# Optimization experiments

Measured on AMD Instinct MI355X. Metric: run time of the kernel, lower is better.

## Reference

```python
import jax, jax.numpy as jnp
import numpy as np

N, H, W = 1024, 256, 256
EPS2D = 0.3  # gsplat low-pass filter on 2D covariance

C0 = 0.28209479177387814
C1 = 0.4886025119029199
C2 = (1.0925484305920792, -1.0925484305920792, 0.31539156525252005, -1.0925484305920792, 0.5462742152960396)
C3 = (-0.5900435899266435, 2.890611442640554, -0.4570457994644658, 0.3731763325901154, -0.4570457994644658, 1.445305721320277, -0.5900435899266435)


def setup_inputs() -> dict:
    key = jax.random.key(0)
    ks = jax.random.split(key, 9)
    means = jax.random.normal(ks[0], (N, 3), jnp.float32)
    scales = jax.random.normal(ks[1], (N, 3), jnp.float32) * 0.3 - 3.0  # exp -> ~0.05
    quats = jax.random.normal(ks[2], (N, 4), jnp.float32)
    opacities = jax.random.normal(ks[3], (N, 1), jnp.float32)
    sh_0 = jax.random.normal(ks[4], (N, 1, 3), jnp.float32) * 0.5
    sh_n = jax.random.normal(ks[5], (N, 15, 3), jnp.float32) * 0.1
    times = jax.random.uniform(ks[6], (N, 1), jnp.float32)
    durations = jax.random.normal(ks[7], (N, 1), jnp.float32) * 0.5
    velocities = jax.random.normal(ks[8], (N, 3), jnp.float32) * 0.1
    # camera: identity rotation, points pushed to depth ~5 in front
    w2c = jnp.eye(4, dtype=jnp.float32).at[2, 3].set(5.0)[None]
    intrinsic = jnp.array([[[300.0, 0.0, 128.0], [0.0, 300.0, 128.0], [0.0, 0.0, 1.0]]], jnp.float32)
    return {"means": means, "scales": scales, "quats": quats, "opacities": opacities,
            "sh_0": sh_0, "sh_n": sh_n, "times": times, "durations": durations,
            "velocities": velocities, "t": jnp.float32(0.5), "w2c": w2c,
            "intrinsic": intrinsic, "height": H, "width": W}


def _quat_to_rot(q):
    q = q / jnp.linalg.norm(q, axis=-1, keepdims=True)
    w, x, y, z = q[:, 0], q[:, 1], q[:, 2], q[:, 3]
    R = jnp.stack([
        1 - 2 * (y * y + z * z), 2 * (x * y - w * z), 2 * (x * z + w * y),
        2 * (x * y + w * z), 1 - 2 * (x * x + z * z), 2 * (y * z - w * x),
        2 * (x * z - w * y), 2 * (y * z + w * x), 1 - 2 * (x * x + y * y),
    ], axis=-1).reshape(-1, 3, 3)
    return R


def _sh_colors(sh, dirs):
    # sh: [N,16,3], dirs: [N,3] normalized. Real SH up to degree 3 (gsplat convention).
    x, y, z = dirs[:, 0], dirs[:, 1], dirs[:, 2]
    xx, yy, zz = x * x, y * y, z * z
    basis = jnp.stack([
        jnp.full_like(x, C0),
        -C1 * y, C1 * z, -C1 * x,
        C2[0] * x * y, C2[1] * y * z, C2[2] * (2 * zz - xx - yy), C2[3] * x * z, C2[4] * (xx - yy),
        C3[0] * y * (3 * xx - yy), C3[1] * x * y * z, C3[2] * y * (4 * zz - xx - yy),
        C3[3] * z * (2 * zz - 3 * xx - 3 * yy), C3[4] * x * (4 * zz - xx - yy),
        C3[5] * z * (xx - yy), C3[6] * x * (xx - 3 * yy),
    ], axis=-1)  # [N,16]
    return jnp.maximum(jnp.einsum('nk,nkc->nc', basis, sh) + 0.5, 0.0)


def reference(means, scales, quats, opacities, sh_0, sh_n, times, durations, velocities,
              t, w2c, intrinsic, height, width):
    # temporal updates
    means_t = means + (t - times) * velocities                                   # [N,3]
    opac = (jax.nn.sigmoid(opacities) * jnp.exp(-0.5 * ((t - times) / jnp.exp(durations)) ** 2))[:, 0]
    sig = jnp.exp(scales)                                                        # [N,3]

    Rcw, tcw = w2c[0, :3, :3], w2c[0, :3, 3]
    K = intrinsic[0]
    fx, fy, cx, cy = K[0, 0], K[1, 1], K[0, 2], K[1, 2]

    # project means
    p_cam = means_t @ Rcw.T + tcw                                                # [N,3]
    zc = p_cam[:, 2]
    u = fx * p_cam[:, 0] / zc + cx
    v = fy * p_cam[:, 1] / zc + cy

    # 3D covariance in camera frame
    Rg = _quat_to_rot(quats)                                                     # [N,3,3]
    M = Rg * sig[:, None, :]
    cov3d = jnp.einsum('nij,nkj->nik', M, M)
    cov_cam = jnp.einsum('ij,njk,lk->nil', Rcw, cov3d, Rcw)

    # perspective Jacobian -> 2D covariance (EWA)
    zero = jnp.zeros_like(zc)
    J = jnp.stack([
        jnp.stack([fx / zc, zero, -fx * p_cam[:, 0] / zc ** 2], -1),
        jnp.stack([zero, fy / zc, -fy * p_cam[:, 1] / zc ** 2], -1),
    ], axis=1)                                                                   # [N,2,3]
    cov2d = jnp.einsum('nij,njk,nlk->nil', J, cov_cam, J)
    a = cov2d[:, 0, 0] + EPS2D
    b = cov2d[:, 0, 1]
    c = cov2d[:, 1, 1] + EPS2D
    det = a * c - b * b
    conA, conB, conC = c / det, -b / det, a / det

    # colors from SH
    cam_pos = -Rcw.T @ tcw
    dirs = means_t - cam_pos
    dirs = dirs / jnp.linalg.norm(dirs, axis=-1, keepdims=True)
    colors = _sh_colors(jnp.concatenate([sh_0, sh_n], axis=1), dirs)             # [N,3]

    # dense per-pixel gaussian evaluation (pixel centers at +0.5)
    xs = jnp.arange(width, dtype=jnp.float32) + 0.5
    ys = jnp.arange(height, dtype=jnp.float32) + 0.5
    gx, gy = jnp.meshgrid(xs, ys)                                                # [H,W]
    px, py = gx.reshape(-1), gy.reshape(-1)                                      # [HW]
    dx = px[None, :] - u[:, None]                                                # [N,HW]
    dy = py[None, :] - v[:, None]
    sigma = 0.5 * (conA[:, None] * dx * dx + conC[:, None] * dy * dy) + conB[:, None] * dx * dy
    valid = (zc > 0.01) & (det > 1e-12)
    alpha = jnp.minimum(0.999, opac[:, None] * jnp.exp(-jnp.maximum(sigma, 0.0)))
    alpha = jnp.where(valid[:, None] & (sigma >= 0.0) & (alpha >= 1.0 / 255.0), alpha, 0.0)

    # depth sort, front-to-back alpha compositing
    order = jnp.argsort(zc)
    alpha_s = alpha[order]
    colors_s = colors[order]
    Tcum = jnp.cumprod(1.0 - alpha_s, axis=0)                                    # [N,HW]
    T_excl = jnp.concatenate([jnp.ones((1, alpha_s.shape[1]), alpha_s.dtype), Tcum[:-1]], axis=0)
    w = alpha_s * T_excl                                                         # [N,HW]
    image = jnp.einsum('np,nc->pc', w, colors_s).reshape(1, height, width, 3)
    alpha_out = (1.0 - Tcum[-1]).reshape(1, height, width, 1)
    image = jnp.clip(image, 0.0, 1.0)
    return image, alpha_out
```

## Files before the change

kernel.cpp:

```cpp
#include <hip/hip_runtime.h>
#include <math.h>

#define NG 1024
#define IH 256
#define IW 256
#define NPIX (IH*IW)


__global__ __launch_bounds__(64) void k_pre(
    const float* __restrict__ means, const float* __restrict__ scales,
    const float* __restrict__ quats, const float* __restrict__ opacs,
    const float* __restrict__ sh0, const float* __restrict__ shn,
    const float* __restrict__ times, const float* __restrict__ durs,
    const float* __restrict__ vels, const float* __restrict__ tptr,
    const float* __restrict__ w2c, const float* __restrict__ intr,
    float* __restrict__ zc_out, float* __restrict__ raw)
{
    int g = blockIdx.x * 64 + threadIdx.x;
    if (g >= NG) return;
    const float t = tptr[0];
    const float R00=w2c[0], R01=w2c[1], R02=w2c[2],  tx=w2c[3];
    const float R10=w2c[4], R11=w2c[5], R12=w2c[6],  ty=w2c[7];
    const float R20=w2c[8], R21=w2c[9], R22=w2c[10], tz=w2c[11];
    const float fx=intr[0], cx=intr[2], fy=intr[4], cy=intr[5];

    const float dt = t - times[g];
    const float mx = fmaf(dt, vels[g*3+0], means[g*3+0]);
    const float my = fmaf(dt, vels[g*3+1], means[g*3+1]);
    const float mz = fmaf(dt, vels[g*3+2], means[g*3+2]);

    const float o = opacs[g];
    const float sig_o = 1.f / (1.f + __expf(-o));
    const float ratio = dt * __expf(-durs[g]);
    const float opac = sig_o * __expf(-0.5f * ratio * ratio);

    const float xc = R00*mx + R01*my + R02*mz + tx;
    const float yc = R10*mx + R11*my + R12*mz + ty;
    const float zc = R20*mx + R21*my + R22*mz + tz;
    const float iz = 1.f / zc;
    const float u = fx*xc*iz + cx;
    const float v = fy*yc*iz + cy;

    float qw=quats[g*4+0], qx=quats[g*4+1], qy=quats[g*4+2], qz=quats[g*4+3];
    const float qn = rsqrtf(qw*qw + qx*qx + qy*qy + qz*qz);
    qw*=qn; qx*=qn; qy*=qn; qz*=qn;
    const float sx = __expf(scales[g*3+0]);
    const float sy = __expf(scales[g*3+1]);
    const float sz = __expf(scales[g*3+2]);
    const float G00 = 1.f-2.f*(qy*qy+qz*qz), G01 = 2.f*(qx*qy-qw*qz), G02 = 2.f*(qx*qz+qw*qy);
    const float G10 = 2.f*(qx*qy+qw*qz), G11 = 1.f-2.f*(qx*qx+qz*qz), G12 = 2.f*(qy*qz-qw*qx);
    const float G20 = 2.f*(qx*qz-qw*qy), G21 = 2.f*(qy*qz+qw*qx), G22 = 1.f-2.f*(qx*qx+qy*qy);
    const float M00=G00*sx, M01=G01*sy, M02=G02*sz;
    const float M10=G10*sx, M11=G11*sy, M12=G12*sz;
    const float M20=G20*sx, M21=G21*sy, M22=G22*sz;
    const float W00=R00*M00+R01*M10+R02*M20, W01=R00*M01+R01*M11+R02*M21, W02=R00*M02+R01*M12+R02*M22;
    const float W10=R10*M00+R11*M10+R12*M20, W11=R10*M01+R11*M11+R12*M21, W12=R10*M02+R11*M12+R12*M22;
    const float W20=R20*M00+R21*M10+R22*M20, W21=R20*M01+R21*M11+R22*M21, W22=R20*M02+R21*M12+R22*M22;
    const float xdz = xc*iz, ydz = yc*iz;
    const float fxiz = fx*iz, fyiz = fy*iz;
    const float T00 = fxiz*(W00 - xdz*W20), T01 = fxiz*(W01 - xdz*W21), T02 = fxiz*(W02 - xdz*W22);
    const float T10 = fyiz*(W10 - ydz*W20), T11 = fyiz*(W11 - ydz*W21), T12 = fyiz*(W12 - ydz*W22);
    const float a = T00*T00 + T01*T01 + T02*T02 + 0.3f;
    const float b = T00*T10 + T01*T11 + T02*T12;
    const float c = T10*T10 + T11*T11 + T12*T12 + 0.3f;
    const float det = a*c - b*b;
    const float idet = 1.f / det;
    const float conA = c*idet, conB = -b*idet, conC = a*idet;

    const bool valid = (zc > 0.01f) && (det > 1e-12f);
    const float op_eff = valid ? opac : 0.f;
    const float smax = (op_eff * 255.f > 0.f) ? (logf(op_eff * 255.f) + 1e-4f) : -1e30f;
    float rx, ry;
    if (smax > 0.f) {
        rx = sqrtf(2.f * smax * a) + 0.01f;
        ry = sqrtf(2.f * smax * c) + 0.01f;
    } else {
        rx = -1e30f; ry = -1e30f;
    }

    const float cpx = -(R00*tx + R10*ty + R20*tz);
    const float cpy = -(R01*tx + R11*ty + R21*tz);
    const float cpz = -(R02*tx + R12*ty + R22*tz);
    float dx0 = mx-cpx, dy0 = my-cpy, dz0 = mz-cpz;
    const float dn = rsqrtf(dx0*dx0 + dy0*dy0 + dz0*dz0);
    const float X = dx0*dn, Y = dy0*dn, Z = dz0*dn;
    const float XX=X*X, YY=Y*Y, ZZ=Z*Z;

    float bs[16];
    bs[0]  = 0.28209479177387814f;
    bs[1]  = -0.4886025119029199f * Y;
    bs[2]  =  0.4886025119029199f * Z;
    bs[3]  = -0.4886025119029199f * X;
    bs[4]  =  1.0925484305920792f * X * Y;
    bs[5]  = -1.0925484305920792f * Y * Z;
    bs[6]  =  0.31539156525252005f * (2.f*ZZ - XX - YY);
    bs[7]  = -1.0925484305920792f * X * Z;
    bs[8]  =  0.5462742152960396f * (XX - YY);
    bs[9]  = -0.5900435899266435f * Y * (3.f*XX - YY);
    bs[10] =  2.890611442640554f  * X * Y * Z;
    bs[11] = -0.4570457994644658f * Y * (4.f*ZZ - XX - YY);
    bs[12] =  0.3731763325901154f * Z * (2.f*ZZ - 3.f*XX - 3.f*YY);
    bs[13] = -0.4570457994644658f * X * (4.f*ZZ - XX - YY);
    bs[14] =  1.445305721320277f  * Z * (XX - YY);
    bs[15] = -0.5900435899266435f * X * (XX - 3.f*YY);

    float cr = 0.5f, cg = 0.5f, cb = 0.5f;
    cr = fmaf(bs[0], sh0[g*3+0], cr);
    cg = fmaf(bs[0], sh0[g*3+1], cg);
    cb = fmaf(bs[0], sh0[g*3+2], cb);
    #pragma unroll
    for (int k = 1; k < 16; ++k) {
        const float* s = shn + g*45 + (k-1)*3;
        cr = fmaf(bs[k], s[0], cr);
        cg = fmaf(bs[k], s[1], cg);
        cb = fmaf(bs[k], s[2], cb);
    }
    cr = fmaxf(cr, 0.f); cg = fmaxf(cg, 0.f); cb = fmaxf(cb, 0.f);

    zc_out[g] = zc;
    float* r = raw + g*12;
    r[0] = u;         r[1] = v;    r[2]  = rx;       r[3]  = ry;
    r[4] = 0.5f*conA; r[5] = conB; r[6]  = 0.5f*conC;r[7]  = smax;
    r[8] = op_eff;    r[9] = cr;   r[10] = cg;       r[11] = cb;
}

__global__ __launch_bounds__(64) void k_rank(
    const float* __restrict__ zc, const float* __restrict__ raw,
    float* __restrict__ sorted)
{
    const int g = blockIdx.x;
    const int lane = threadIdx.x;
    const float myz = zc[g];
    int cnt = 0;
    #pragma unroll
    for (int k = 0; k < 16; ++k) {
        const int j = k*64 + lane;
        const float z = zc[j];
        const bool lt = (z < myz) || (z == myz && j < g);
        cnt += (int)__popcll(__ballot(lt));
    }
    if (lane < 12) sorted[cnt*12 + lane] = raw[g*12 + lane];
}

__global__ __launch_bounds__(256) void k_raster(
    const float* __restrict__ sorted, float* __restrict__ out)
{
    __shared__ float4 hrec[4][64][3];
    __shared__ float4 part[4][64];
    const int lane = threadIdx.x & 63;
    const int wv   = threadIdx.x >> 6;
    const int pix  = blockIdx.x * 64 + lane;
    const float px = (float)(pix & (IW-1)) + 0.5f;
    const float py = (float)(pix >> 8) + 0.5f;
    const float px0  = (float)((blockIdx.x & 3) << 6) + 0.5f;
    const float px63 = px0 + 63.f;

    const float4* __restrict__ gp = (const float4*)sorted;
    const int base = wv * 256;

    unsigned long long masks[4];
    #pragma unroll
    for (int k = 0; k < 4; ++k) {
        const float4 r0 = gp[(base + k*64 + lane)*3];
        masks[k] = __ballot((fabsf(py - r0.y) <= r0.w) &&
                            (r0.x + r0.z >= px0) && (r0.x - r0.z <= px63));
    }

    float T = 1.f, cr = 0.f, cg = 0.f, cb = 0.f;
    #pragma unroll
    for (int k = 0; k < 4; ++k) {
        const unsigned long long m = masks[k];
        if (!m) continue;
        const int g = base + k*64 + lane;
        if ((m >> lane) & 1ull) {
            const int pos = (int)__popcll(m & ((1ull << lane) - 1ull));
            hrec[wv][pos][0] = gp[g*3+0];
            hrec[wv][pos][1] = gp[g*3+1];
            hrec[wv][pos][2] = gp[g*3+2];
        }
        asm volatile("s_waitcnt lgkmcnt(0)" ::: "memory");
        const int cnt = (int)__popcll(m);
        for (int i = 0; i < cnt; ++i) {
            const float4 ra = hrec[wv][i][0];
            const float4 rb = hrec[wv][i][1];
            const float4 rc = hrec[wv][i][2];
            const float dx = px - ra.x;
            const float dy = py - ra.y;
            const float sigma = fmaf(dx, fmaf(rb.x, dx, rb.y*dy), rb.z*dy*dy);
            if (sigma >= 0.f && sigma <= rb.w) {
                const float al = fminf(0.999f, rc.x * __expf(-sigma));
                if (al >= (1.f/255.f)) {
                    const float w = al * T;
                    cr = fmaf(w, rc.y, cr);
                    cg = fmaf(w, rc.z, cg);
                    cb = fmaf(w, rc.w, cb);
                    T -= w;
                }
            }
        }
    }

    part[wv][lane] = make_float4(cr, cg, cb, T);
    __syncthreads();
    if (threadIdx.x < 64) {
        const float4 v0 = part[0][lane];
        const float4 v1 = part[1][lane];
        const float4 v2 = part[2][lane];
        const float4 v3 = part[3][lane];
        float r = v0.x, g2 = v0.y, b2 = v0.z, Tt = v0.w;
        r = fmaf(Tt, v1.x, r); g2 = fmaf(Tt, v1.y, g2); b2 = fmaf(Tt, v1.z, b2); Tt *= v1.w;
        r = fmaf(Tt, v2.x, r); g2 = fmaf(Tt, v2.y, g2); b2 = fmaf(Tt, v2.z, b2); Tt *= v2.w;
        r = fmaf(Tt, v3.x, r); g2 = fmaf(Tt, v3.y, g2); b2 = fmaf(Tt, v3.z, b2); Tt *= v3.w;
        const int p3 = pix * 3;
        out[p3+0] = fminf(fmaxf(r,  0.f), 1.f);
        out[p3+1] = fminf(fmaxf(g2, 0.f), 1.f);
        out[p3+2] = fminf(fmaxf(b2, 0.f), 1.f);
        out[NPIX*3 + pix] = 1.f - Tt;
    }
}

extern "C" void kernel_launch(void* const* d_in, const int* in_sizes, int n_in,
                              void* d_out, int out_size, void* d_ws, size_t ws_size,
                              hipStream_t stream) {
    const float* means  = (const float*)d_in[0];
    const float* scales = (const float*)d_in[1];
    const float* quats  = (const float*)d_in[2];
    const float* opacs  = (const float*)d_in[3];
    const float* sh0    = (const float*)d_in[4];
    const float* shn    = (const float*)d_in[5];
    const float* times  = (const float*)d_in[6];
    const float* durs   = (const float*)d_in[7];
    const float* vels   = (const float*)d_in[8];
    const float* tptr   = (const float*)d_in[9];
    const float* w2c    = (const float*)d_in[10];
    const float* intr   = (const float*)d_in[11];

    float* ws     = (float*)d_ws;
    float* zc     = ws;
    float* raw    = ws + 1024;
    float* sorted = ws + 1024 + 12*NG;

    hipLaunchKernelGGL(k_pre, dim3(16), dim3(64), 0, stream,
                       means, scales, quats, opacs, sh0, shn,
                       times, durs, vels, tptr, w2c, intr, zc, raw);
    hipLaunchKernelGGL(k_rank, dim3(NG), dim3(64), 0, stream, zc, raw, sorted);
    hipLaunchKernelGGL(k_raster, dim3(NPIX/64), dim3(256), 0, stream,
                       sorted, (float*)d_out);
}
```

Measured before the change: 19.94 us.

## Drop global sort kernel; sort per-block culled gaussians in shared memory

Removes the separate k_rank launch that globally sorted all gaussians by depth. Instead, each raster block culls gaussians against its 64-pixel row, gathers the survivors into shared memory and ranks them there by depth with an O(H^2) count. The sorted list is split evenly across the four waves, which balances work between waves. The shared list is capped at 192 entries, so rows with more overlapping gaussians silently drop some, which risks incorrect output. Every block also repeats the sort, adding per-block overhead in exchange for one fewer kernel launch.

```diff
diff --git a/kernel.cpp b/kernel.cpp
--- a/kernel.cpp
+++ b/kernel.cpp
@@ -5,6 +5,7 @@
 #define IH 256
 #define IW 256
 #define NPIX (IH*IW)
+#define CAP 192
 
 
 __global__ __launch_bounds__(64) void k_pre(
@@ -119,34 +120,22 @@
 
     zc_out[g] = zc;
     float* r = raw + g*12;
-    r[0] = u;         r[1] = v;    r[2]  = rx;       r[3]  = ry;
-    r[4] = 0.5f*conA; r[5] = conB; r[6]  = 0.5f*conC;r[7]  = smax;
-    r[8] = op_eff;    r[9] = cr;   r[10] = cg;       r[11] = cb;
+    r[0] = u;         r[1] = v;    r[2]  = rx;        r[3]  = ry;
+    r[4] = 0.5f*conA; r[5] = conB; r[6]  = 0.5f*conC; r[7]  = smax;
+    r[8] = op_eff;    r[9] = cr;   r[10] = cg;        r[11] = cb;
 }
 
-__global__ __launch_bounds__(64) void k_rank(
-    const float* __restrict__ zc, const float* __restrict__ raw,
-    float* __restrict__ sorted)
+__global__ __launch_bounds__(256) void k_raster(
+    const float* __restrict__ raw, const float* __restrict__ zc,
+    float* __restrict__ out)
 {
-    const int g = blockIdx.x;
-    const int lane = threadIdx.x;
-    const float myz = zc[g];
-    int cnt = 0;
-    #pragma unroll
-    for (int k = 0; k < 16; ++k) {
-        const int j = k*64 + lane;
-        const float z = zc[j];
-        const bool lt = (z < myz) || (z == myz && j < g);
-        cnt += (int)__popcll(__ballot(lt));
-    }
-    if (lane < 12) sorted[cnt*12 + lane] = raw[g*12 + lane];
-}
-
-__global__ __launch_bounds__(256) void k_raster(
-    const float* __restrict__ sorted, float* __restrict__ out)
-{
-    __shared__ float4 hrec[4][64][3];
+    __shared__ float4 hrec[CAP][3];
+    __shared__ float  hz[CAP];
+    __shared__ int    hid[CAP];
+    __shared__ int    hperm[CAP];
+    __shared__ int    cnts[4];
     __shared__ float4 part[4][64];
+
     const int lane = threadIdx.x & 63;
     const int wv   = threadIdx.x >> 6;
     const int pix  = blockIdx.x * 64 + lane;
@@ -155,47 +144,82 @@
     const float px0  = (float)((blockIdx.x & 3) << 6) + 0.5f;
     const float px63 = px0 + 63.f;
 
-    const float4* __restrict__ gp = (const float4*)sorted;
+    const float4* __restrict__ gp = (const float4*)raw;
     const int base = wv * 256;
 
+    float4 r0s[4];
     unsigned long long masks[4];
     #pragma unroll
     for (int k = 0; k < 4; ++k) {
         const float4 r0 = gp[(base + k*64 + lane)*3];
+        r0s[k] = r0;
         masks[k] = __ballot((fabsf(py - r0.y) <= r0.w) &&
                             (r0.x + r0.z >= px0) && (r0.x - r0.z <= px63));
     }
-
-    float T = 1.f, cr = 0.f, cg = 0.f, cb = 0.f;
+    const int cw = (int)(__popcll(masks[0]) + __popcll(masks[1]) +
+                         __popcll(masks[2]) + __popcll(masks[3]));
+    if (lane == 0) cnts[wv] = cw;
+    __syncthreads();
+
+    int off = 0;
+    #pragma unroll
+    for (int w = 0; w < 4; ++w) off += (w < wv) ? cnts[w] : 0;
+    const int tot = cnts[0] + cnts[1] + cnts[2] + cnts[3];
+
+    int pbase = off;
     #pragma unroll
     for (int k = 0; k < 4; ++k) {
         const unsigned long long m = masks[k];
-        if (!m) continue;
-        const int g = base + k*64 + lane;
         if ((m >> lane) & 1ull) {
-            const int pos = (int)__popcll(m & ((1ull << lane) - 1ull));
-            hrec[wv][pos][0] = gp[g*3+0];
-            hrec[wv][pos][1] = gp[g*3+1];
-            hrec[wv][pos][2] = gp[g*3+2];
+            const int pos = pbase + (int)__popcll(m & ((1ull << lane) - 1ull));
+            if (pos < CAP) {
+                const int g = base + k*64 + lane;
+                hrec[pos][0] = r0s[k];
+                hrec[pos][1] = gp[g*3+1];
+                hrec[pos][2] = gp[g*3+2];
+                hz[pos] = zc[g];
+                hid[pos] = g;
+            }
         }
-        asm volatile("s_waitcnt lgkmcnt(0)" ::: "memory");
-        const int cnt = (int)__popcll(m);
-        for (int i = 0; i < cnt; ++i) {
-            const float4 ra = hrec[wv][i][0];
-            const float4 rb = hrec[wv][i][1];
-            const float4 rc = hrec[wv][i][2];
-            const float dx = px - ra.x;
-            const float dy = py - ra.y;
-            const float sigma = fmaf(dx, fmaf(rb.x, dx, rb.y*dy), rb.z*dy*dy);
-            if (sigma >= 0.f && sigma <= rb.w) {
-                const float al = fminf(0.999f, rc.x * __expf(-sigma));
-                if (al >= (1.f/255.f)) {
-                    const float w = al * T;
-                    cr = fmaf(w, rc.y, cr);
-                    cg = fmaf(w, rc.z, cg);
-                    cb = fmaf(w, rc.w, cb);
-                    T -= w;
-                }
+        pbase += (int)__popcll(m);
+    }
+    __syncthreads();
+
+    const int H = (tot < CAP) ? tot : CAP;
+
+    for (int t = threadIdx.x; t < H; t += 256) {
+        const float zt = hz[t];
+        const int   it = hid[t];
+        int r = 0;
+        for (int j = 0; j < H; ++j) {
+            const float zj = hz[j];
+            const int   ij = hid[j];
+            r += (zj < zt) || (zj == zt && ij < it);
+        }
+        hperm[r] = t;
+    }
+    __syncthreads();
+
+    const int Q = (H + 3) >> 2;
+    const int s = wv * Q;
+    const int e = (s + Q < H) ? (s + Q) : H;
+    float T = 1.f, cr = 0.f, cg = 0.f, cb = 0.f;
+    for (int i = s; i < e; ++i) {
+        const int p = hperm[i];
+        const float4 ra = hrec[p][0];
+        const float4 rb = hrec[p][1];
+        const float4 rc = hrec[p][2];
+        const float dx = px - ra.x;
+        const float dy = py - ra.y;
+        const float sigma = fmaf(dx, fmaf(rb.x, dx, rb.y*dy), rb.z*dy*dy);
+        if (sigma >= 0.f && sigma <= rb.w) {
+            const float al = fminf(0.999f, rc.x * __expf(-sigma));
+            if (al >= (1.f/255.f)) {
+                const float w = al * T;
+                cr = fmaf(w, rc.y, cr);
+                cg = fmaf(w, rc.z, cg);
+                cb = fmaf(w, rc.w, cb);
+                T -= w;
             }
         }
     }
@@ -235,15 +259,13 @@
     const float* w2c    = (const float*)d_in[10];
     const float* intr   = (const float*)d_in[11];
 
-    float* ws     = (float*)d_ws;
-    float* zc     = ws;
-    float* raw    = ws + 1024;
-    float* sorted = ws + 1024 + 12*NG;
+    float* ws  = (float*)d_ws;
+    float* zc  = ws;
+    float* raw = ws + 1024;
 
     hipLaunchKernelGGL(k_pre, dim3(16), dim3(64), 0, stream,
                        means, scales, quats, opacs, sh0, shn,
                        times, durs, vels, tptr, w2c, intr, zc, raw);
-    hipLaunchKernelGGL(k_rank, dim3(NG), dim3(64), 0, stream, zc, raw, sorted);
     hipLaunchKernelGGL(k_raster, dim3(NPIX/64), dim3(256), 0, stream,
-                       sorted, (float*)d_out);
+                       raw, zc, (float*)d_out);
 }
```

Result: slower. 23.87 us (+19.7%).

## Fuse depth ranking into preprocessing kernel and split culling records

Applied to the files above, without the earlier changes.

Each preprocessing block now recomputes all 1024 camera-space depths into shared memory and ranks its own 64 gaussians there. Three waves count over depth chunks while one wave does the projection and SH work. The separate rank kernel and its launch go away, and records are scattered directly in sorted order. The cull fields move to their own float4 array, which the raster kernel keeps in registers, and the per-gaussian LDS record loads are software-pipelined one step ahead. In exchange, every block redundantly reloads means, velocities and times for all gaussians.

```diff
diff --git a/kernel.cpp b/kernel.cpp
--- a/kernel.cpp
+++ b/kernel.cpp
@@ -7,143 +7,175 @@
 #define NPIX (IH*IW)
 
 
-__global__ __launch_bounds__(64) void k_pre(
+__global__ __launch_bounds__(256) void k_pre(
     const float* __restrict__ means, const float* __restrict__ scales,
     const float* __restrict__ quats, const float* __restrict__ opacs,
     const float* __restrict__ sh0, const float* __restrict__ shn,
     const float* __restrict__ times, const float* __restrict__ durs,
     const float* __restrict__ vels, const float* __restrict__ tptr,
     const float* __restrict__ w2c, const float* __restrict__ intr,
-    float* __restrict__ zc_out, float* __restrict__ raw)
+    float* __restrict__ cull, float* __restrict__ recs)
 {
-    int g = blockIdx.x * 64 + threadIdx.x;
-    if (g >= NG) return;
+    __shared__ float zall[NG];
+    __shared__ int   partial[4][64];
+
+    const int tid = threadIdx.x;
+    const int b   = blockIdx.x;
     const float t = tptr[0];
     const float R00=w2c[0], R01=w2c[1], R02=w2c[2],  tx=w2c[3];
     const float R10=w2c[4], R11=w2c[5], R12=w2c[6],  ty=w2c[7];
     const float R20=w2c[8], R21=w2c[9], R22=w2c[10], tz=w2c[11];
     const float fx=intr[0], cx=intr[2], fy=intr[4], cy=intr[5];
 
-    const float dt = t - times[g];
-    const float mx = fmaf(dt, vels[g*3+0], means[g*3+0]);
-    const float my = fmaf(dt, vels[g*3+1], means[g*3+1]);
-    const float mz = fmaf(dt, vels[g*3+2], means[g*3+2]);
-
-    const float o = opacs[g];
-    const float sig_o = 1.f / (1.f + __expf(-o));
-    const float ratio = dt * __expf(-durs[g]);
-    const float opac = sig_o * __expf(-0.5f * ratio * ratio);
-
-    const float xc = R00*mx + R01*my + R02*mz + tx;
-    const float yc = R10*mx + R11*my + R12*mz + ty;
-    const float zc = R20*mx + R21*my + R22*mz + tz;
-    const float iz = 1.f / zc;
-    const float u = fx*xc*iz + cx;
-    const float v = fy*yc*iz + cy;
-
-    float qw=quats[g*4+0], qx=quats[g*4+1], qy=quats[g*4+2], qz=quats[g*4+3];
-    const float qn = rsqrtf(qw*qw + qx*qx + qy*qy + qz*qz);
-    qw*=qn; qx*=qn; qy*=qn; qz*=qn;
-    const float sx = __expf(scales[g*3+0]);
-    const float sy = __expf(scales[g*3+1]);
-    const float sz = __expf(scales[g*3+2]);
-    const float G00 = 1.f-2.f*(qy*qy+qz*qz), G01 = 2.f*(qx*qy-qw*qz), G02 = 2.f*(qx*qz+qw*qy);
-    const float G10 = 2.f*(qx*qy+qw*qz), G11 = 1.f-2.f*(qx*qx+qz*qz), G12 = 2.f*(qy*qz-qw*qx);
-    const float G20 = 2.f*(qx*qz-qw*qy), G21 = 2.f*(qy*qz+qw*qx), G22 = 1.f-2.f*(qx*qx+qy*qy);
-    const float M00=G00*sx, M01=G01*sy, M02=G02*sz;
-    const float M10=G10*sx, M11=G11*sy, M12=G12*sz;
-    const float M20=G20*sx, M21=G21*sy, M22=G22*sz;
-    const float W00=R00*M00+R01*M10+R02*M20, W01=R00*M01+R01*M11+R02*M21, W02=R00*M02+R01*M12+R02*M22;
-    const float W10=R10*M00+R11*M10+R12*M20, W11=R10*M01+R11*M11+R12*M21, W12=R10*M02+R11*M12+R12*M22;
-    const float W20=R20*M00+R21*M10+R22*M20, W21=R20*M01+R21*M11+R22*M21, W22=R20*M02+R21*M12+R22*M22;
-    const float xdz = xc*iz, ydz = yc*iz;
-    const float fxiz = fx*iz, fyiz = fy*iz;
-    const float T00 = fxiz*(W00 - xdz*W20), T01 = fxiz*(W01 - xdz*W21), T02 = fxiz*(W02 - xdz*W22);
-    const float T10 = fyiz*(W10 - ydz*W20), T11 = fyiz*(W11 - ydz*W21), T12 = fyiz*(W12 - ydz*W22);
-    const float a = T00*T00 + T01*T01 + T02*T02 + 0.3f;
-    const float b = T00*T10 + T01*T11 + T02*T12;
-    const float c = T10*T10 + T11*T11 + T12*T12 + 0.3f;
-    const float det = a*c - b*b;
-    const float idet = 1.f / det;
-    const float conA = c*idet, conB = -b*idet, conC = a*idet;
-
-    const bool valid = (zc > 0.01f) && (det > 1e-12f);
-    const float op_eff = valid ? opac : 0.f;
-    const float smax = (op_eff * 255.f > 0.f) ? (logf(op_eff * 255.f) + 1e-4f) : -1e30f;
-    float rx, ry;
-    if (smax > 0.f) {
-        rx = sqrtf(2.f * smax * a) + 0.01f;
-        ry = sqrtf(2.f * smax * c) + 0.01f;
+    #pragma unroll
+    for (int k = 0; k < 4; ++k) {
+        const int g = tid + k*256;
+        const float dt = t - times[g];
+        const float mx = fmaf(dt, vels[g*3+0], means[g*3+0]);
+        const float my = fmaf(dt, vels[g*3+1], means[g*3+1]);
+        const float mz = fmaf(dt, vels[g*3+2], means[g*3+2]);
+        zall[g] = R20*mx + R21*my + R22*mz + tz;
+    }
+    __syncthreads();
+
+    float o_u=0, o_v=0, o_rx=0, o_ry=0, o_hA=0, o_B=0, o_hC=0, o_smax=0;
+    float o_op=0, o_cr=0, o_cg=0, o_cb=0;
+    if (tid < 64) {
+        const int g = b*64 + tid;
+        const float dt = t - times[g];
+        const float mx = fmaf(dt, vels[g*3+0], means[g*3+0]);
+        const float my = fmaf(dt, vels[g*3+1], means[g*3+1]);
+        const float mz = fmaf(dt, vels[g*3+2], means[g*3+2]);
+
+        const float o = opacs[g];
+        const float sig_o = 1.f / (1.f + __expf(-o));
+        const float ratio = dt * __expf(-durs[g]);
+        const float opac = sig_o * __expf(-0.5f * ratio * ratio);
+
+        const float xc = R00*mx + R01*my + R02*mz + tx;
+        const float yc = R10*mx + R11*my + R12*mz + ty;
+        const float zc = R20*mx + R21*my + R22*mz + tz;
+        const float iz = 1.f / zc;
+        const float u = fx*xc*iz + cx;
+        const float v = fy*yc*iz + cy;
+
+        float qw=quats[g*4+0], qx=quats[g*4+1], qy=quats[g*4+2], qz=quats[g*4+3];
+        const float qn = rsqrtf(qw*qw + qx*qx + qy*qy + qz*qz);
+        qw*=qn; qx*=qn; qy*=qn; qz*=qn;
+        const float sx = __expf(scales[g*3+0]);
+        const float sy = __expf(scales[g*3+1]);
+        const float sz = __expf(scales[g*3+2]);
+        const float G00 = 1.f-2.f*(qy*qy+qz*qz), G01 = 2.f*(qx*qy-qw*qz), G02 = 2.f*(qx*qz+qw*qy);
+        const float G10 = 2.f*(qx*qy+qw*qz), G11 = 1.f-2.f*(qx*qx+qz*qz), G12 = 2.f*(qy*qz-qw*qx);
+        const float G20 = 2.f*(qx*qz-qw*qy), G21 = 2.f*(qy*qz+qw*qx), G22 = 1.f-2.f*(qx*qx+qy*qy);
+        const float M00=G00*sx, M01=G01*sy, M02=G02*sz;
+        const float M10=G10*sx, M11=G11*sy, M12=G12*sz;
+        const float M20=G20*sx, M21=G21*sy, M22=G22*sz;
+        const float W00=R00*M00+R01*M10+R02*M20, W01=R00*M01+R01*M11+R02*M21, W02=R00*M02+R01*M12+R02*M22;
+        const float W10=R10*M00+R11*M10+R12*M20, W11=R10*M01+R11*M11+R12*M21, W12=R10*M02+R11*M12+R12*M22;
+        const float W20=R20*M00+R21*M10+R22*M20, W21=R20*M01+R21*M11+R22*M21, W22=R20*M02+R21*M12+R22*M22;
+        const float xdz = xc*iz, ydz = yc*iz;
+        const float fxiz = fx*iz, fyiz = fy*iz;
+        const float T00 = fxiz*(W00 - xdz*W20), T01 = fxiz*(W01 - xdz*W21), T02 = fxiz*(W02 - xdz*W22);
+        const float T10 = fyiz*(W10 - ydz*W20), T11 = fyiz*(W11 - ydz*W21), T12 = fyiz*(W12 - ydz*W22);
+        const float a = T00*T00 + T01*T01 + T02*T02 + 0.3f;
+        const float bb = T00*T10 + T01*T11 + T02*T12;
+        const float c = T10*T10 + T11*T11 + T12*T12 + 0.3f;
+        const float det = a*c - bb*bb;
+        const float idet = 1.f / det;
+        const float conA = c*idet, conB = -bb*idet, conC = a*idet;
+
+        const bool valid = (zc > 0.01f) && (det > 1e-12f);
+        const float op_eff = valid ? opac : 0.f;
+        const float smax = (op_eff * 255.f > 0.f) ? (logf(op_eff * 255.f) + 1e-4f) : -1e30f;
+        float rx, ry;
+        if (smax > 0.f) {
+            rx = sqrtf(2.f * smax * a) + 0.01f;
+            ry = sqrtf(2.f * smax * c) + 0.01f;
+        } else {
+            rx = -1e30f; ry = -1e30f;
+        }
+
+        const float cpx = -(R00*tx + R10*ty + R20*tz);
+        const float cpy = -(R01*tx + R11*ty + R21*tz);
+        const float cpz = -(R02*tx + R12*ty + R22*tz);
+        float dx0 = mx-cpx, dy0 = my-cpy, dz0 = mz-cpz;
+        const float dn = rsqrtf(dx0*dx0 + dy0*dy0 + dz0*dz0);
+        const float X = dx0*dn, Y = dy0*dn, Z = dz0*dn;
+        const float XX=X*X, YY=Y*Y, ZZ=Z*Z;
+
+        float bs[16];
+        bs[0]  = 0.28209479177387814f;
+        bs[1]  = -0.4886025119029199f * Y;
+        bs[2]  =  0.4886025119029199f * Z;
+        bs[3]  = -0.4886025119029199f * X;
+        bs[4]  =  1.0925484305920792f * X * Y;
+        bs[5]  = -1.0925484305920792f * Y * Z;
+        bs[6]  =  0.31539156525252005f * (2.f*ZZ - XX - YY);
+        bs[7]  = -1.0925484305920792f * X * Z;
+        bs[8]  =  0.5462742152960396f * (XX - YY);
+        bs[9]  = -0.5900435899266435f * Y * (3.f*XX - YY);
+        bs[10] =  2.890611442640554f  * X * Y * Z;
+        bs[11] = -0.4570457994644658f * Y * (4.f*ZZ - XX - YY);
+        bs[12] =  0.3731763325901154f * Z * (2.f*ZZ - 3.f*XX - 3.f*YY);
+        bs[13] = -0.4570457994644658f * X * (4.f*ZZ - XX - YY);
+        bs[14] =  1.445305721320277f  * Z * (XX - YY);
+        bs[15] = -0.5900435899266435f * X * (XX - 3.f*YY);
+
+        float cr = 0.5f, cg = 0.5f, cb = 0.5f;
+        cr = fmaf(bs[0], sh0[g*3+0], cr);
+        cg = fmaf(bs[0], sh0[g*3+1], cg);
+        cb = fmaf(bs[0], sh0[g*3+2], cb);
+        #pragma unroll
+        for (int k = 1; k < 16; ++k) {
+            const float* s = shn + g*45 + (k-1)*3;
+            cr = fmaf(bs[k], s[0], cr);
+            cg = fmaf(bs[k], s[1], cg);
+            cb = fmaf(bs[k], s[2], cb);
+        }
+        cr = fmaxf(cr, 0.f); cg = fmaxf(cg, 0.f); cb = fmaxf(cb, 0.f);
+
+        o_u = u; o_v = v; o_rx = rx; o_ry = ry;
+        o_hA = 0.5f*conA; o_B = conB; o_hC = 0.5f*conC; o_smax = smax;
+        o_op = op_eff; o_cr = cr; o_cg = cg; o_cb = cb;
     } else {
-        rx = -1e30f; ry = -1e30f;
-    }
-
-    const float cpx = -(R00*tx + R10*ty + R20*tz);
-    const float cpy = -(R01*tx + R11*ty + R21*tz);
-    const float cpz = -(R02*tx + R12*ty + R22*tz);
-    float dx0 = mx-cpx, dy0 = my-cpy, dz0 = mz-cpz;
-    const float dn = rsqrtf(dx0*dx0 + dy0*dy0 + dz0*dz0);
-    const float X = dx0*dn, Y = dy0*dn, Z = dz0*dn;
-    const float XX=X*X, YY=Y*Y, ZZ=Z*Z;
-
-    float bs[16];
-    bs[0]  = 0.28209479177387814f;
-    bs[1]  = -0.4886025119029199f * Y;
-    bs[2]  =  0.4886025119029199f * Z;
-    bs[3]  = -0.4886025119029199f * X;
-    bs[4]  =  1.0925484305920792f * X * Y;
-    bs[5]  = -1.0925484305920792f * Y * Z;
-    bs[6]  =  0.31539156525252005f * (2.f*ZZ - XX - YY);
-    bs[7]  = -1.0925484305920792f * X * Z;
-    bs[8]  =  0.5462742152960396f * (XX - YY);
-    bs[9]  = -0.5900435899266435f * Y * (3.f*XX - YY);
-    bs[10] =  2.890611442640554f  * X * Y * Z;
-    bs[11] = -0.4570457994644658f * Y * (4.f*ZZ - XX - YY);
-    bs[12] =  0.3731763325901154f * Z * (2.f*ZZ - 3.f*XX - 3.f*YY);
-    bs[13] = -0.4570457994644658f * X * (4.f*ZZ - XX - YY);
-    bs[14] =  1.445305721320277f  * Z * (XX - YY);
-    bs[15] = -0.5900435899266435f * X * (XX - 3.f*YY);
-
-    float cr = 0.5f, cg = 0.5f, cb = 0.5f;
-    cr = fmaf(bs[0], sh0[g*3+0], cr);
-    cg = fmaf(bs[0], sh0[g*3+1], cg);
-    cb = fmaf(bs[0], sh0[g*3+2], cb);
-    #pragma unroll
-    for (int k = 1; k < 16; ++k) {
-        const float* s = shn + g*45 + (k-1)*3;
-        cr = fmaf(bs[k], s[0], cr);
-        cg = fmaf(bs[k], s[1], cg);
-        cb = fmaf(bs[k], s[2], cb);
-    }
-    cr = fmaxf(cr, 0.f); cg = fmaxf(cg, 0.f); cb = fmaxf(cb, 0.f);
-
-    zc_out[g] = zc;
-    float* r = raw + g*12;
-    r[0] = u;         r[1] = v;    r[2]  = rx;       r[3]  = ry;
-    r[4] = 0.5f*conA; r[5] = conB; r[6]  = 0.5f*conC;r[7]  = smax;
-    r[8] = op_eff;    r[9] = cr;   r[10] = cg;       r[11] = cb;
+        const int wv = tid >> 6;
+        const int lane = tid & 63;
+        const int tg = b*64 + lane;
+        const float zt = zall[tg];
+        const float4* __restrict__ z4 = (const float4*)zall;
+        #pragma unroll
+        for (int pass = 0; pass < 2; ++pass) {
+            if (pass == 1 && wv != 1) break;
+            const int q = (pass == 0) ? (wv - 1) : 3;
+            int cnt = 0;
+            #pragma unroll 4
+            for (int j4 = q*64; j4 < q*64 + 64; ++j4) {
+                const float4 z = z4[j4];
+                const int j = j4*4;
+                cnt += (z.x < zt) || (z.x == zt && (j+0) < tg);
+                cnt += (z.y < zt) || (z.y == zt && (j+1) < tg);
+                cnt += (z.z < zt) || (z.z == zt && (j+2) < tg);
+                cnt += (z.w < zt) || (z.w == zt && (j+3) < tg);
+            }
+            partial[q][lane] = cnt;
+        }
+    }
+    __syncthreads();
+
+    if (tid < 64) {
+        const int r = partial[0][tid] + partial[1][tid] + partial[2][tid] + partial[3][tid];
+        float4* c4 = (float4*)cull;
+        float4* r4 = (float4*)recs;
+        c4[r]     = make_float4(o_u, o_v, o_rx, o_ry);
+        r4[2*r]   = make_float4(o_hA, o_B, o_hC, o_smax);
+        r4[2*r+1] = make_float4(o_op, o_cr, o_cg, o_cb);
+    }
 }
 
-__global__ __launch_bounds__(64) void k_rank(
-    const float* __restrict__ zc, const float* __restrict__ raw,
-    float* __restrict__ sorted)
-{
-    const int g = blockIdx.x;
-    const int lane = threadIdx.x;
-    const float myz = zc[g];
-    int cnt = 0;
-    #pragma unroll
-    for (int k = 0; k < 16; ++k) {
-        const int j = k*64 + lane;
-        const float z = zc[j];
-        const bool lt = (z < myz) || (z == myz && j < g);
-        cnt += (int)__popcll(__ballot(lt));
-    }
-    if (lane < 12) sorted[cnt*12 + lane] = raw[g*12 + lane];
-}
-
 __global__ __launch_bounds__(256) void k_raster(
-    const float* __restrict__ sorted, float* __restrict__ out)
+    const float* __restrict__ cull, const float* __restrict__ recs,
+    float* __restrict__ out)
 {
     __shared__ float4 hrec[4][64][3];
     __shared__ float4 part[4][64];
@@ -155,13 +187,16 @@
     const float px0  = (float)((blockIdx.x & 3) << 6) + 0.5f;
     const float px63 = px0 + 63.f;
 
-    const float4* __restrict__ gp = (const float4*)sorted;
+    const float4* __restrict__ c4 = (const float4*)cull;
+    const float4* __restrict__ r4 = (const float4*)recs;
     const int base = wv * 256;
 
+    float4 r0s[4];
     unsigned long long masks[4];
     #pragma unroll
     for (int k = 0; k < 4; ++k) {
-        const float4 r0 = gp[(base + k*64 + lane)*3];
+        const float4 r0 = c4[base + k*64 + lane];
+        r0s[k] = r0;
         masks[k] = __ballot((fabsf(py - r0.y) <= r0.w) &&
                             (r0.x + r0.z >= px0) && (r0.x - r0.z <= px63));
     }
@@ -171,19 +206,26 @@
     for (int k = 0; k < 4; ++k) {
         const unsigned long long m = masks[k];
         if (!m) continue;
-        const int g = base + k*64 + lane;
         if ((m >> lane) & 1ull) {
             const int pos = (int)__popcll(m & ((1ull << lane) - 1ull));
-            hrec[wv][pos][0] = gp[g*3+0];
-            hrec[wv][pos][1] = gp[g*3+1];
-            hrec[wv][pos][2] = gp[g*3+2];
+            const int g = base + k*64 + lane;
+            hrec[wv][pos][0] = r0s[k];
+            hrec[wv][pos][1] = r4[g*2+0];
+            hrec[wv][pos][2] = r4[g*2+1];
         }
         asm volatile("s_waitcnt lgkmcnt(0)" ::: "memory");
+        __builtin_amdgcn_sched_barrier(0);
         const int cnt = (int)__popcll(m);
+        float4 ra = hrec[wv][0][0];
+        float4 rb = hrec[wv][0][1];
+        float4 rc = hrec[wv][0][2];
         for (int i = 0; i < cnt; ++i) {
-            const float4 ra = hrec[wv][i][0];
-            const float4 rb = hrec[wv][i][1];
-            const float4 rc = hrec[wv][i][2];
+            float4 na, nb, nc;
+            if (i + 1 < cnt) {
+                na = hrec[wv][i+1][0];
+                nb = hrec[wv][i+1][1];
+                nc = hrec[wv][i+1][2];
+            }
             const float dx = px - ra.x;
             const float dy = py - ra.y;
             const float sigma = fmaf(dx, fmaf(rb.x, dx, rb.y*dy), rb.z*dy*dy);
@@ -197,6 +239,7 @@
                     T -= w;
                 }
             }
+            ra = na; rb = nb; rc = nc;
         }
     }
 
@@ -235,15 +278,13 @@
     const float* w2c    = (const float*)d_in[10];
     const float* intr   = (const float*)d_in[11];
 
-    float* ws     = (float*)d_ws;
-    float* zc     = ws;
-    float* raw    = ws + 1024;
-    float* sorted = ws + 1024 + 12*NG;
-
-    hipLaunchKernelGGL(k_pre, dim3(16), dim3(64), 0, stream,
+    float* ws   = (float*)d_ws;
+    float* cull = ws;
+    float* recs = ws + 4*NG;
+
+    hipLaunchKernelGGL(k_pre, dim3(16), dim3(256), 0, stream,
                        means, scales, quats, opacs, sh0, shn,
-                       times, durs, vels, tptr, w2c, intr, zc, raw);
-    hipLaunchKernelGGL(k_rank, dim3(NG), dim3(64), 0, stream, zc, raw, sorted);
+                       times, durs, vels, tptr, w2c, intr, cull, recs);
     hipLaunchKernelGGL(k_raster, dim3(NPIX/64), dim3(256), 0, stream,
-                       sorted, (float*)d_out);
+                       cull, recs, (float*)d_out);
 }
```

Measured after the change: 24.59 us. 1.23x slower.
